# Kernel tuning notes

Hardware: AMD Instinct MI355X
Metric: run time of the kernel (lower is better)

Reference implementation:

```python
import jax, jax.numpy as jnp
import numpy as np

B, N, H, A, S = 8, 8192, 256, 64, 32  # batch, nodes, hidden, annotation, sub_graphs


def _mysoftmax(x):
    # exp, zero out where x <= 0, normalize over last dim, nan (0/0) -> 0
    x_exp = jnp.where(x > 0, jnp.exp(x), 0.0)
    part = jnp.sum(x_exp, axis=-1, keepdims=True)
    # safe divide: where partition == 0 the faithful result after nan_to_num is 0
    return jnp.where(part > 0, x_exp / jnp.where(part > 0, part, 1.0), 0.0)


def setup_inputs() -> dict:
    key = jax.random.key(0)
    k1, k2, k3, k4, k5, k6 = jax.random.split(key, 6)
    x = jax.random.normal(k1, (B, N, H + A), dtype=jnp.float32)
    node_map = jax.random.uniform(k2, (B, S, N), dtype=jnp.float32)
    lim = 1.0 / np.sqrt(H + A)
    Wi = jax.random.uniform(k3, (H, H + A), minval=-lim, maxval=lim, dtype=jnp.float32)
    bi = jax.random.uniform(k4, (H,), minval=-lim, maxval=lim, dtype=jnp.float32)
    Wj = jax.random.uniform(k5, (H, H + A), minval=-lim, maxval=lim, dtype=jnp.float32)
    bj = jax.random.uniform(k6, (H,), minval=-lim, maxval=lim, dtype=jnp.float32)
    return {"x": x, "node_map": node_map, "Wi": Wi, "bi": bi, "Wj": Wj, "bj": bj}


def reference(x, node_map, Wi, bi, Wj, bj):
    # gated node features: sigmoid(fc_i(x)) * tanh(fc_j(x))  -> [B, N, H]
    x_sigm = jax.nn.sigmoid(jnp.einsum('bnf,hf->bnh', x, Wi) + bi)
    x_tanh = jnp.tanh(jnp.einsum('bnf,hf->bnh', x, Wj) + bj)
    x_all = x_sigm * x_tanh
    # per-node L2 norm -> [B, 1, N]
    x_norm = jnp.linalg.norm(x_all, axis=-1)[:, None, :]
    # scaled subgraph map and masked softmax over nodes -> [B, S, N]
    weight = _mysoftmax(node_map * x_norm)
    # weighted sum over nodes (replaces [B,S,N,H] broadcast) -> [B, S, H]
    pooled = jnp.einsum('bsn,bnh->bsh', weight, x_all)
    return jnp.tanh(pooled), weight[..., None]
```

## Files before the change

### kernel.cpp

```cpp
#include <hip/hip_runtime.h>
#include <cstdint>
#include <cstddef>

typedef unsigned short u16;
typedef unsigned int   u32;
using short8 = __attribute__((ext_vector_type(8))) short;
using f32x4  = __attribute__((ext_vector_type(4))) float;

#define NB    8
#define NN    8192
#define HH    256
#define FF    320
#define SS    32
#define NROWS 65536
#define NCH   64

__device__ __forceinline__ u16 f2bf(float f) {
    union { float f; u32 u; } v; v.f = f;
    u32 r = v.u + 0x7fffu + ((v.u >> 16) & 1u);
    return (u16)(r >> 16);
}
__device__ __forceinline__ u32 pk2h(float lo, float hi) {
    union { float f; u32 u; } a, b; a.f = lo; b.f = hi;
    return __builtin_amdgcn_perm(b.u + 0x8000u, a.u + 0x8000u, 0x07060302u);
}
__device__ __forceinline__ short8 pack8(float4 a, float4 b) {
    union { u32 u[4]; short8 s; } r;
    r.u[0] = pk2h(a.x, a.y); r.u[1] = pk2h(a.z, a.w);
    r.u[2] = pk2h(b.x, b.y); r.u[3] = pk2h(b.z, b.w);
    return r.s;
}

__global__ __launch_bounds__(256) void prep_w(const float* __restrict__ Wi,
                                              const float* __restrict__ Wj,
                                              u16* __restrict__ Wb,
                                              float* __restrict__ normsq) {
    int idx = blockIdx.x * 256 + threadIdx.x;
    float v = (idx < 81920) ? Wi[idx] : Wj[idx - 81920];
    Wb[idx] = f2bf(v);
    if (idx < NROWS) normsq[idx] = 0.f;
}

__global__ __launch_bounds__(512, 4) void gemm_gate(
    const float* __restrict__ x, const u16* __restrict__ Wb,
    const float* __restrict__ bi, const float* __restrict__ bj,
    u16* __restrict__ xa, float* __restrict__ normsq)
{
    __shared__ u16 lB[5 * 8192];

    const int bx   = blockIdx.x;
    const int xcd  = bx & 7;
    const int ht   = (bx >> 3) & 3;
    const int slot = bx >> 5;
    const int mb   = xcd + slot * 8;
    const int m0   = mb * 256;
    const int h0   = ht * 64;
    const int b_idx = m0 >> 13;
    const int n0    = m0 & 8191;

    const int tid  = threadIdx.x;
    const int w    = tid >> 6;
    const int lane = tid & 63;
    const int quad = lane >> 4;
    const int l15  = lane & 15;

    {
        const int rsub = lane >> 3;
        const int kg   = (lane & 7) ^ rsub;
        #pragma unroll
        for (int kt = 0; kt < 5; ++kt) {
            #pragma unroll
            for (int j = 0; j < 2; ++j) {
                int sl  = w * 2 + j;
                int row = sl * 8 + rsub;
                int mat = row >> 6, hl = row & 63;
                const u16* gsrc = Wb + mat * 81920 + (size_t)(h0 + hl) * FF + kt * 64 + kg * 8;
                u16* ldst = &lB[kt * 8192 + sl * 512];
                __builtin_amdgcn_global_load_lds(
                    (const __attribute__((address_space(1))) void*)gsrc,
                    (__attribute__((address_space(3))) void*)ldst, 16, 0, 0);
            }
        }
    }

    const float* xb = x + (size_t)(m0 + w * 32 + l15) * FF + quad * 8;

    f32x4 acc[8][2];
    #pragma unroll
    for (int a = 0; a < 8; ++a)
        #pragma unroll
        for (int m = 0; m < 2; ++m) acc[a][m] = (f32x4){0.f, 0.f, 0.f, 0.f};

    float4 pre[3][2][2];
    #pragma unroll
    for (int s = 0; s < 2; ++s)
        #pragma unroll
        for (int mt = 0; mt < 2; ++mt) {
            pre[s][mt][0] = *reinterpret_cast<const float4*>(xb + mt * 16 * FF + s * 32);
            pre[s][mt][1] = *reinterpret_cast<const float4*>(xb + mt * 16 * FF + s * 32 + 4);
        }

    __syncthreads();

    #pragma unroll
    for (int ks = 0; ks < 10; ++ks) {
        const int kt  = ks >> 1, kk = ks & 1;
        const int cur = ks % 3;
        if (ks < 8) {
            const int nx = (ks + 2) % 3;
            const int f  = (ks + 2) * 32;
            #pragma unroll
            for (int mt = 0; mt < 2; ++mt) {
                pre[nx][mt][0] = *reinterpret_cast<const float4*>(xb + mt * 16 * FF + f);
                pre[nx][mt][1] = *reinterpret_cast<const float4*>(xb + mt * 16 * FF + f + 4);
            }
        }
        short8 af0 = pack8(pre[cur][0][0], pre[cur][0][1]);
        short8 af1 = pack8(pre[cur][1][0], pre[cur][1][1]);
        #pragma unroll
        for (int mn = 0; mn < 8; ++mn) {
            int c = mn * 16 + l15;
            short8 bv = *reinterpret_cast<const short8*>(
                &lB[kt * 8192 + c * 64 + (((kk * 4 + quad) ^ (c & 7)) << 3)]);
            acc[mn][0] = __builtin_amdgcn_mfma_f32_16x16x32_bf16(af0, bv, acc[mn][0], 0, 0, 0);
            acc[mn][1] = __builtin_amdgcn_mfma_f32_16x16x32_bf16(af1, bv, acc[mn][1], 0, 0, 0);
        }
    }

    float s0[2][4];
    #pragma unroll
    for (int mt = 0; mt < 2; ++mt)
        #pragma unroll
        for (int r = 0; r < 4; ++r) s0[mt][r] = 0.f;

    #pragma unroll
    for (int hq = 0; hq < 4; ++hq) {
        int h = h0 + hq * 16 + l15;
        float bi_v = bi[h], bj_v = bj[h];
        #pragma unroll
        for (int mt = 0; mt < 2; ++mt) {
            float xall[4];
            #pragma unroll
            for (int r = 0; r < 4; ++r) {
                float yi = acc[hq][mt][r] + bi_v;
                float yj = acc[hq + 4][mt][r] + bj_v;
                float sg = 1.f / (1.f + __expf(-yi));
                float e2 = __expf(-2.f * yj);
                float th = (1.f - e2) / (1.f + e2);
                float xv = sg * th;
                xall[r] = xv;
                s0[mt][r] += xv * xv;
            }
            uint2 pk;
            pk.x = pk2h(xall[0], xall[1]);
            pk.y = pk2h(xall[2], xall[3]);
            size_t o = (size_t)b_idx * ((size_t)HH * NN) + (size_t)h * NN
                     + (size_t)(n0 + w * 32 + mt * 16 + quad * 4);
            *reinterpret_cast<uint2*>(&xa[o]) = pk;
        }
    }
    #pragma unroll
    for (int m = 1; m <= 8; m <<= 1) {
        #pragma unroll
        for (int mt = 0; mt < 2; ++mt)
            #pragma unroll
            for (int r = 0; r < 4; ++r)
                s0[mt][r] += __shfl_xor(s0[mt][r], m, 64);
    }
    if (l15 == 0) {
        #pragma unroll
        for (int mt = 0; mt < 2; ++mt)
            #pragma unroll
            for (int r = 0; r < 4; ++r)
                atomicAdd(&normsq[m0 + w * 32 + mt * 16 + quad * 4 + r], s0[mt][r]);
    }
}

__global__ __launch_bounds__(1024) void softmax_k(
    const float* __restrict__ nm, const float* __restrict__ normsq,
    float* __restrict__ out1)
{
    __shared__ float red[16];
    int bs = blockIdx.x;
    int b  = bs >> 5;
    const float* src = nm + (size_t)bs * NN;
    float* dst       = out1 + (size_t)bs * NN;
    const float* ns  = normsq + (size_t)b * NN;
    int tid = threadIdx.x;
    float e[8];
    float sum = 0.f;
    #pragma unroll
    for (int i = 0; i < 8; ++i) {
        int n = i * 1024 + tid;
        float logit = src[n] * sqrtf(ns[n]);
        float v = (logit > 0.f) ? __expf(logit) : 0.f;
        e[i] = v;
        sum += v;
    }
    #pragma unroll
    for (int m = 1; m <= 32; m <<= 1) sum += __shfl_xor(sum, m, 64);
    int w = tid >> 6, lane = tid & 63;
    if (lane == 0) red[w] = sum;
    __syncthreads();
    float part = 0.f;
    #pragma unroll
    for (int j = 0; j < 16; ++j) part += red[j];
    float inv = (part > 0.f) ? (1.f / part) : 0.f;
    #pragma unroll
    for (int i = 0; i < 8; ++i) dst[i * 1024 + tid] = e[i] * inv;
}

__global__ __launch_bounds__(256) void pooled_k(
    const u16* __restrict__ xa, const float* __restrict__ wgt,
    float* __restrict__ part)
{
    __shared__ u16 lw[32 * 136];
    int bx = blockIdx.x;
    int b  = bx >> 6, c = bx & 63;
    int n0 = c * 128;
    int tid = threadIdx.x, w = tid >> 6, lane = tid & 63, quad = lane >> 4, l15 = lane & 15;

    const u16* ab = xa + (size_t)b * ((size_t)HH * NN) + n0;

    short8 av[2][4];
    #pragma unroll
    for (int htl = 0; htl < 4; ++htl) {
        int h = w * 64 + htl * 16 + l15;
        av[0][htl] = *reinterpret_cast<const short8*>(ab + (size_t)h * NN + quad * 8);
    }

    {
        int s  = tid >> 3;
        int jq = (tid & 7) * 16;
        const float* src = wgt + (size_t)(b * SS + s) * NN + n0 + jq;
        #pragma unroll
        for (int q = 0; q < 4; ++q) {
            float4 v = *reinterpret_cast<const float4*>(src + q * 4);
            uint2 pk;
            pk.x = pk2h(v.x, v.y);
            pk.y = pk2h(v.z, v.w);
            *reinterpret_cast<uint2*>(&lw[s * 136 + jq + q * 4]) = pk;
        }
    }
    __syncthreads();

    f32x4 acc[4][2];
    #pragma unroll
    for (int a = 0; a < 4; ++a)
        #pragma unroll
        for (int s = 0; s < 2; ++s) acc[a][s] = (f32x4){0.f, 0.f, 0.f, 0.f};

    #pragma unroll
    for (int ks = 0; ks < 4; ++ks) {
        const int cur = ks & 1, nxt = cur ^ 1;
        if (ks < 3) {
            #pragma unroll
            for (int htl = 0; htl < 4; ++htl) {
                int h = w * 64 + htl * 16 + l15;
                av[nxt][htl] = *reinterpret_cast<const short8*>(
                    ab + (size_t)h * NN + (ks + 1) * 32 + quad * 8);
            }
        }
        #pragma unroll
        for (int st = 0; st < 2; ++st) {
            int s = st * 16 + l15;
            short8 bv = *reinterpret_cast<const short8*>(&lw[s * 136 + ks * 32 + quad * 8]);
            #pragma unroll
            for (int htl = 0; htl < 4; ++htl)
                acc[htl][st] = __builtin_amdgcn_mfma_f32_16x16x32_bf16(av[cur][htl], bv, acc[htl][st], 0, 0, 0);
        }
    }
    float* pb = part + (size_t)(b * NCH + c) * 8192;
    #pragma unroll
    for (int htl = 0; htl < 4; ++htl) {
        #pragma unroll
        for (int st = 0; st < 2; ++st) {
            int h = w * 64 + htl * 16 + quad * 4;
            int s = st * 16 + l15;
            *reinterpret_cast<f32x4*>(&pb[s * 256 + h]) = acc[htl][st];
        }
    }
}

__global__ __launch_bounds__(256) void reduce_tanh(const float* __restrict__ part,
                                                   float* __restrict__ out0)
{
    int gid = blockIdx.x * 256 + threadIdx.x;
    int b = gid >> 13, r = gid & 8191;
    const float* p = part + (size_t)b * NCH * 8192 + r;
    float s = 0.f;
    #pragma unroll
    for (int c = 0; c < NCH; ++c) s += p[(size_t)c * 8192];
    out0[gid] = tanhf(s);
}

extern "C" void kernel_launch(void* const* d_in, const int* in_sizes, int n_in,
                              void* d_out, int out_size, void* d_ws, size_t ws_size,
                              hipStream_t stream) {
    const float* x  = (const float*)d_in[0];
    const float* nm = (const float*)d_in[1];
    const float* Wi = (const float*)d_in[2];
    const float* bi = (const float*)d_in[3];
    const float* Wj = (const float*)d_in[4];
    const float* bj = (const float*)d_in[5];
    float* out0 = (float*)d_out;
    float* out1 = out0 + NB * SS * HH;

    char* ws = (char*)d_ws;
    u16*   Wb     = (u16*)ws;
    u16*   xa     = (u16*)(ws + 327680);
    float* normsq = (float*)(ws + 327680 + 33554432);
    float* part   = (float*)(ws + 327680 + 33554432 + 262144);

    prep_w     <<<640,  256, 0, stream>>>(Wi, Wj, Wb, normsq);
    gemm_gate  <<<1024, 512, 0, stream>>>(x, Wb, bi, bj, xa, normsq);
    softmax_k  <<<256, 1024, 0, stream>>>(nm, normsq, out1);
    pooled_k   <<<512,  256, 0, stream>>>(xa, out1, part);
    reduce_tanh<<<256,  256, 0, stream>>>(part, out0);
}
```

Before: 214.9 us.

## Double gemm M-tile per block and replace normsq atomics with per-tile partials

Each gemm block now computes 512 rows instead of 256 (4 M sub-tiles per wave), halving the grid and the number of times each block reloads the weight tile into LDS. This raises reuse of each B fragment read from LDS across four MFMAs. The per-row squared-norm is written as four per-h-tile partials instead of atomics, and softmax sums them, which also removes the zeroing pass in prep_w. The cost is higher register pressure from doubled accumulators and prefetch buffers, possibly lowering occupancy. The partial buffer reuses the pooled partial workspace, which is safe only because softmax finishes before pooled_k writes it.

```diff
diff --git a/kernel.cpp b/kernel.cpp
--- a/kernel.cpp
+++ b/kernel.cpp
@@ -33,18 +33,16 @@
 
 __global__ __launch_bounds__(256) void prep_w(const float* __restrict__ Wi,
                                               const float* __restrict__ Wj,
-                                              u16* __restrict__ Wb,
-                                              float* __restrict__ normsq) {
+                                              u16* __restrict__ Wb) {
     int idx = blockIdx.x * 256 + threadIdx.x;
     float v = (idx < 81920) ? Wi[idx] : Wj[idx - 81920];
     Wb[idx] = f2bf(v);
-    if (idx < NROWS) normsq[idx] = 0.f;
 }
 
 __global__ __launch_bounds__(512, 4) void gemm_gate(
     const float* __restrict__ x, const u16* __restrict__ Wb,
     const float* __restrict__ bi, const float* __restrict__ bj,
-    u16* __restrict__ xa, float* __restrict__ normsq)
+    u16* __restrict__ xa, float* __restrict__ normsq_p)
 {
     __shared__ u16 lB[5 * 8192];
 
@@ -53,7 +51,7 @@
     const int ht   = (bx >> 3) & 3;
     const int slot = bx >> 5;
     const int mb   = xcd + slot * 8;
-    const int m0   = mb * 256;
+    const int m0   = mb * 512;
     const int h0   = ht * 64;
     const int b_idx = m0 >> 13;
     const int n0    = m0 & 8191;
@@ -83,19 +81,19 @@
         }
     }
 
-    const float* xb = x + (size_t)(m0 + w * 32 + l15) * FF + quad * 8;
-
-    f32x4 acc[8][2];
+    const float* xb = x + (size_t)(m0 + w * 64 + l15) * FF + quad * 8;
+
+    f32x4 acc[8][4];
     #pragma unroll
     for (int a = 0; a < 8; ++a)
         #pragma unroll
-        for (int m = 0; m < 2; ++m) acc[a][m] = (f32x4){0.f, 0.f, 0.f, 0.f};
-
-    float4 pre[3][2][2];
+        for (int m = 0; m < 4; ++m) acc[a][m] = (f32x4){0.f, 0.f, 0.f, 0.f};
+
+    float4 pre[3][4][2];
     #pragma unroll
     for (int s = 0; s < 2; ++s)
         #pragma unroll
-        for (int mt = 0; mt < 2; ++mt) {
+        for (int mt = 0; mt < 4; ++mt) {
             pre[s][mt][0] = *reinterpret_cast<const float4*>(xb + mt * 16 * FF + s * 32);
             pre[s][mt][1] = *reinterpret_cast<const float4*>(xb + mt * 16 * FF + s * 32 + 4);
         }
@@ -110,26 +108,29 @@
             const int nx = (ks + 2) % 3;
             const int f  = (ks + 2) * 32;
             #pragma unroll
-            for (int mt = 0; mt < 2; ++mt) {
+            for (int mt = 0; mt < 4; ++mt) {
                 pre[nx][mt][0] = *reinterpret_cast<const float4*>(xb + mt * 16 * FF + f);
                 pre[nx][mt][1] = *reinterpret_cast<const float4*>(xb + mt * 16 * FF + f + 4);
             }
         }
-        short8 af0 = pack8(pre[cur][0][0], pre[cur][0][1]);
-        short8 af1 = pack8(pre[cur][1][0], pre[cur][1][1]);
+        short8 af[4];
+        #pragma unroll
+        for (int mt = 0; mt < 4; ++mt)
+            af[mt] = pack8(pre[cur][mt][0], pre[cur][mt][1]);
         #pragma unroll
         for (int mn = 0; mn < 8; ++mn) {
             int c = mn * 16 + l15;
             short8 bv = *reinterpret_cast<const short8*>(
                 &lB[kt * 8192 + c * 64 + (((kk * 4 + quad) ^ (c & 7)) << 3)]);
-            acc[mn][0] = __builtin_amdgcn_mfma_f32_16x16x32_bf16(af0, bv, acc[mn][0], 0, 0, 0);
-            acc[mn][1] = __builtin_amdgcn_mfma_f32_16x16x32_bf16(af1, bv, acc[mn][1], 0, 0, 0);
-        }
-    }
-
-    float s0[2][4];
-    #pragma unroll
-    for (int mt = 0; mt < 2; ++mt)
+            #pragma unroll
+            for (int mt = 0; mt < 4; ++mt)
+                acc[mn][mt] = __builtin_amdgcn_mfma_f32_16x16x32_bf16(af[mt], bv, acc[mn][mt], 0, 0, 0);
+        }
+    }
+
+    float s0[4][4];
+    #pragma unroll
+    for (int mt = 0; mt < 4; ++mt)
         #pragma unroll
         for (int r = 0; r < 4; ++r) s0[mt][r] = 0.f;
 
@@ -138,7 +139,7 @@
         int h = h0 + hq * 16 + l15;
         float bi_v = bi[h], bj_v = bj[h];
         #pragma unroll
-        for (int mt = 0; mt < 2; ++mt) {
+        for (int mt = 0; mt < 4; ++mt) {
             float xall[4];
             #pragma unroll
             for (int r = 0; r < 4; ++r) {
@@ -155,29 +156,29 @@
             pk.x = pk2h(xall[0], xall[1]);
             pk.y = pk2h(xall[2], xall[3]);
             size_t o = (size_t)b_idx * ((size_t)HH * NN) + (size_t)h * NN
-                     + (size_t)(n0 + w * 32 + mt * 16 + quad * 4);
+                     + (size_t)(n0 + w * 64 + mt * 16 + quad * 4);
             *reinterpret_cast<uint2*>(&xa[o]) = pk;
         }
     }
     #pragma unroll
     for (int m = 1; m <= 8; m <<= 1) {
         #pragma unroll
-        for (int mt = 0; mt < 2; ++mt)
+        for (int mt = 0; mt < 4; ++mt)
             #pragma unroll
             for (int r = 0; r < 4; ++r)
                 s0[mt][r] += __shfl_xor(s0[mt][r], m, 64);
     }
     if (l15 == 0) {
         #pragma unroll
-        for (int mt = 0; mt < 2; ++mt)
+        for (int mt = 0; mt < 4; ++mt)
             #pragma unroll
             for (int r = 0; r < 4; ++r)
-                atomicAdd(&normsq[m0 + w * 32 + mt * 16 + quad * 4 + r], s0[mt][r]);
+                normsq_p[ht * NROWS + m0 + w * 64 + mt * 16 + quad * 4 + r] = s0[mt][r];
     }
 }
 
 __global__ __launch_bounds__(1024) void softmax_k(
-    const float* __restrict__ nm, const float* __restrict__ normsq,
+    const float* __restrict__ nm, const float* __restrict__ normsq_p,
     float* __restrict__ out1)
 {
     __shared__ float red[16];
@@ -185,14 +186,15 @@
     int b  = bs >> 5;
     const float* src = nm + (size_t)bs * NN;
     float* dst       = out1 + (size_t)bs * NN;
-    const float* ns  = normsq + (size_t)b * NN;
+    const float* ns  = normsq_p + (size_t)b * NN;
     int tid = threadIdx.x;
     float e[8];
     float sum = 0.f;
     #pragma unroll
     for (int i = 0; i < 8; ++i) {
         int n = i * 1024 + tid;
-        float logit = src[n] * sqrtf(ns[n]);
+        float nsq = ns[n] + ns[n + NROWS] + ns[n + 2 * NROWS] + ns[n + 3 * NROWS];
+        float logit = src[n] * sqrtf(nsq);
         float v = (logit > 0.f) ? __expf(logit) : 0.f;
         e[i] = v;
         sum += v;
@@ -307,14 +309,14 @@
     float* out1 = out0 + NB * SS * HH;
 
     char* ws = (char*)d_ws;
-    u16*   Wb     = (u16*)ws;
-    u16*   xa     = (u16*)(ws + 327680);
-    float* normsq = (float*)(ws + 327680 + 33554432);
-    float* part   = (float*)(ws + 327680 + 33554432 + 262144);
-
-    prep_w     <<<640,  256, 0, stream>>>(Wi, Wj, Wb, normsq);
-    gemm_gate  <<<1024, 512, 0, stream>>>(x, Wb, bi, bj, xa, normsq);
-    softmax_k  <<<256, 1024, 0, stream>>>(nm, normsq, out1);
+    u16*   Wb       = (u16*)ws;
+    u16*   xa       = (u16*)(ws + 327680);
+    float* part     = (float*)(ws + 327680 + 33554432);
+    float* normsq_p = part;
+
+    prep_w     <<<640,  256, 0, stream>>>(Wi, Wj, Wb);
+    gemm_gate  <<<512,  512, 0, stream>>>(x, Wb, bi, bj, xa, normsq_p);
+    softmax_k  <<<256, 1024, 0, stream>>>(nm, normsq_p, out1);
     pooled_k   <<<512,  256, 0, stream>>>(xa, out1, part);
     reduce_tanh<<<256,  256, 0, stream>>>(part, out0);
 }
```

After: 502.4 us. 2.34x slower.

## Pre-cast x to bf16 in a separate pass and replace norm atomics with partial sums

Applied to the files above, without the earlier changes.

Adds a cast_x kernel that converts x to bf16 in workspace so the GEMM reads half-width A operands, with a deeper prefetch ring and no per-tile packing. The squared-norm accumulation becomes per-h-tile partial stores that softmax sums, which removes the atomics and the zeroing in prep_w. The extra pass costs a full read of x plus a bf16 write and reread. It runs only when the workspace is large enough; otherwise an fp32-input fallback GEMM is used.

```diff
diff --git a/kernel.cpp b/kernel.cpp
--- a/kernel.cpp
+++ b/kernel.cpp
@@ -33,18 +33,28 @@
 
 __global__ __launch_bounds__(256) void prep_w(const float* __restrict__ Wi,
                                               const float* __restrict__ Wj,
-                                              u16* __restrict__ Wb,
-                                              float* __restrict__ normsq) {
+                                              u16* __restrict__ Wb) {
     int idx = blockIdx.x * 256 + threadIdx.x;
     float v = (idx < 81920) ? Wi[idx] : Wj[idx - 81920];
     Wb[idx] = f2bf(v);
-    if (idx < NROWS) normsq[idx] = 0.f;
-}
-
-__global__ __launch_bounds__(512, 4) void gemm_gate(
-    const float* __restrict__ x, const u16* __restrict__ Wb,
+}
+
+__global__ __launch_bounds__(256) void cast_x(const float* __restrict__ x,
+                                              u16* __restrict__ xb) {
+    int t = blockIdx.x * 256 + threadIdx.x;
+    #pragma unroll
+    for (int i = 0; i < 4; ++i) {
+        size_t g = (size_t)i * 655360 + t;
+        float4 a = *reinterpret_cast<const float4*>(x + g * 8);
+        float4 b = *reinterpret_cast<const float4*>(x + g * 8 + 4);
+        *reinterpret_cast<short8*>(xb + g * 8) = pack8(a, b);
+    }
+}
+
+__global__ __launch_bounds__(512, 4) void gemm_gate_pre(
+    const u16* __restrict__ xbg, const u16* __restrict__ Wb,
     const float* __restrict__ bi, const float* __restrict__ bj,
-    u16* __restrict__ xa, float* __restrict__ normsq)
+    u16* __restrict__ xa, float* __restrict__ normsq_p)
 {
     __shared__ u16 lB[5 * 8192];
 
@@ -83,7 +93,8 @@
         }
     }
 
-    const float* xb = x + (size_t)(m0 + w * 32 + l15) * FF + quad * 8;
+    const u16* xr0 = xbg + (size_t)(m0 + w * 32 + l15) * FF + quad * 8;
+    const u16* xr1 = xr0 + 16 * FF;
 
     f32x4 acc[8][2];
     #pragma unroll
@@ -91,39 +102,31 @@
         #pragma unroll
         for (int m = 0; m < 2; ++m) acc[a][m] = (f32x4){0.f, 0.f, 0.f, 0.f};
 
-    float4 pre[3][2][2];
-    #pragma unroll
-    for (int s = 0; s < 2; ++s)
-        #pragma unroll
-        for (int mt = 0; mt < 2; ++mt) {
-            pre[s][mt][0] = *reinterpret_cast<const float4*>(xb + mt * 16 * FF + s * 32);
-            pre[s][mt][1] = *reinterpret_cast<const float4*>(xb + mt * 16 * FF + s * 32 + 4);
-        }
+    short8 af[4][2];
+    #pragma unroll
+    for (int s = 0; s < 3; ++s) {
+        af[s][0] = *reinterpret_cast<const short8*>(xr0 + s * 32);
+        af[s][1] = *reinterpret_cast<const short8*>(xr1 + s * 32);
+    }
 
     __syncthreads();
 
     #pragma unroll
     for (int ks = 0; ks < 10; ++ks) {
         const int kt  = ks >> 1, kk = ks & 1;
-        const int cur = ks % 3;
-        if (ks < 8) {
-            const int nx = (ks + 2) % 3;
-            const int f  = (ks + 2) * 32;
-            #pragma unroll
-            for (int mt = 0; mt < 2; ++mt) {
-                pre[nx][mt][0] = *reinterpret_cast<const float4*>(xb + mt * 16 * FF + f);
-                pre[nx][mt][1] = *reinterpret_cast<const float4*>(xb + mt * 16 * FF + f + 4);
-            }
-        }
-        short8 af0 = pack8(pre[cur][0][0], pre[cur][0][1]);
-        short8 af1 = pack8(pre[cur][1][0], pre[cur][1][1]);
+        const int cur = ks & 3;
+        if (ks < 7) {
+            const int nx = (ks + 3) & 3;
+            af[nx][0] = *reinterpret_cast<const short8*>(xr0 + (ks + 3) * 32);
+            af[nx][1] = *reinterpret_cast<const short8*>(xr1 + (ks + 3) * 32);
+        }
         #pragma unroll
         for (int mn = 0; mn < 8; ++mn) {
             int c = mn * 16 + l15;
             short8 bv = *reinterpret_cast<const short8*>(
                 &lB[kt * 8192 + c * 64 + (((kk * 4 + quad) ^ (c & 7)) << 3)]);
-            acc[mn][0] = __builtin_amdgcn_mfma_f32_16x16x32_bf16(af0, bv, acc[mn][0], 0, 0, 0);
-            acc[mn][1] = __builtin_amdgcn_mfma_f32_16x16x32_bf16(af1, bv, acc[mn][1], 0, 0, 0);
+            acc[mn][0] = __builtin_amdgcn_mfma_f32_16x16x32_bf16(af[cur][0], bv, acc[mn][0], 0, 0, 0);
+            acc[mn][1] = __builtin_amdgcn_mfma_f32_16x16x32_bf16(af[cur][1], bv, acc[mn][1], 0, 0, 0);
         }
     }
 
@@ -172,12 +175,147 @@
         for (int mt = 0; mt < 2; ++mt)
             #pragma unroll
             for (int r = 0; r < 4; ++r)
-                atomicAdd(&normsq[m0 + w * 32 + mt * 16 + quad * 4 + r], s0[mt][r]);
+                normsq_p[ht * NROWS + m0 + w * 32 + mt * 16 + quad * 4 + r] = s0[mt][r];
+    }
+}
+
+__global__ __launch_bounds__(512, 4) void gemm_gate_f32(
+    const float* __restrict__ x, const u16* __restrict__ Wb,
+    const float* __restrict__ bi, const float* __restrict__ bj,
+    u16* __restrict__ xa, float* __restrict__ normsq_p)
+{
+    __shared__ u16 lB[5 * 8192];
+
+    const int bx   = blockIdx.x;
+    const int xcd  = bx & 7;
+    const int ht   = (bx >> 3) & 3;
+    const int slot = bx >> 5;
+    const int mb   = xcd + slot * 8;
+    const int m0   = mb * 256;
+    const int h0   = ht * 64;
+    const int b_idx = m0 >> 13;
+    const int n0    = m0 & 8191;
+
+    const int tid  = threadIdx.x;
+    const int w    = tid >> 6;
+    const int lane = tid & 63;
+    const int quad = lane >> 4;
+    const int l15  = lane & 15;
+
+    {
+        const int rsub = lane >> 3;
+        const int kg   = (lane & 7) ^ rsub;
+        #pragma unroll
+        for (int kt = 0; kt < 5; ++kt) {
+            #pragma unroll
+            for (int j = 0; j < 2; ++j) {
+                int sl  = w * 2 + j;
+                int row = sl * 8 + rsub;
+                int mat = row >> 6, hl = row & 63;
+                const u16* gsrc = Wb + mat * 81920 + (size_t)(h0 + hl) * FF + kt * 64 + kg * 8;
+                u16* ldst = &lB[kt * 8192 + sl * 512];
+                __builtin_amdgcn_global_load_lds(
+                    (const __attribute__((address_space(1))) void*)gsrc,
+                    (__attribute__((address_space(3))) void*)ldst, 16, 0, 0);
+            }
+        }
+    }
+
+    const float* xb = x + (size_t)(m0 + w * 32 + l15) * FF + quad * 8;
+
+    f32x4 acc[8][2];
+    #pragma unroll
+    for (int a = 0; a < 8; ++a)
+        #pragma unroll
+        for (int m = 0; m < 2; ++m) acc[a][m] = (f32x4){0.f, 0.f, 0.f, 0.f};
+
+    float4 pre[3][2][2];
+    #pragma unroll
+    for (int s = 0; s < 2; ++s)
+        #pragma unroll
+        for (int mt = 0; mt < 2; ++mt) {
+            pre[s][mt][0] = *reinterpret_cast<const float4*>(xb + mt * 16 * FF + s * 32);
+            pre[s][mt][1] = *reinterpret_cast<const float4*>(xb + mt * 16 * FF + s * 32 + 4);
+        }
+
+    __syncthreads();
+
+    #pragma unroll
+    for (int ks = 0; ks < 10; ++ks) {
+        const int kt  = ks >> 1, kk = ks & 1;
+        const int cur = ks % 3;
+        if (ks < 8) {
+            const int nx = (ks + 2) % 3;
+            const int f  = (ks + 2) * 32;
+            #pragma unroll
+            for (int mt = 0; mt < 2; ++mt) {
+                pre[nx][mt][0] = *reinterpret_cast<const float4*>(xb + mt * 16 * FF + f);
+                pre[nx][mt][1] = *reinterpret_cast<const float4*>(xb + mt * 16 * FF + f + 4);
+            }
+        }
+        short8 af0 = pack8(pre[cur][0][0], pre[cur][0][1]);
+        short8 af1 = pack8(pre[cur][1][0], pre[cur][1][1]);
+        #pragma unroll
+        for (int mn = 0; mn < 8; ++mn) {
+            int c = mn * 16 + l15;
+            short8 bv = *reinterpret_cast<const short8*>(
+                &lB[kt * 8192 + c * 64 + (((kk * 4 + quad) ^ (c & 7)) << 3)]);
+            acc[mn][0] = __builtin_amdgcn_mfma_f32_16x16x32_bf16(af0, bv, acc[mn][0], 0, 0, 0);
+            acc[mn][1] = __builtin_amdgcn_mfma_f32_16x16x32_bf16(af1, bv, acc[mn][1], 0, 0, 0);
+        }
+    }
+
+    float s0[2][4];
+    #pragma unroll
+    for (int mt = 0; mt < 2; ++mt)
+        #pragma unroll
+        for (int r = 0; r < 4; ++r) s0[mt][r] = 0.f;
+
+    #pragma unroll
+    for (int hq = 0; hq < 4; ++hq) {
+        int h = h0 + hq * 16 + l15;
+        float bi_v = bi[h], bj_v = bj[h];
+        #pragma unroll
+        for (int mt = 0; mt < 2; ++mt) {
+            float xall[4];
+            #pragma unroll
+            for (int r = 0; r < 4; ++r) {
+                float yi = acc[hq][mt][r] + bi_v;
+                float yj = acc[hq + 4][mt][r] + bj_v;
+                float sg = 1.f / (1.f + __expf(-yi));
+                float e2 = __expf(-2.f * yj);
+                float th = (1.f - e2) / (1.f + e2);
+                float xv = sg * th;
+                xall[r] = xv;
+                s0[mt][r] += xv * xv;
+            }
+            uint2 pk;
+            pk.x = pk2h(xall[0], xall[1]);
+            pk.y = pk2h(xall[2], xall[3]);
+            size_t o = (size_t)b_idx * ((size_t)HH * NN) + (size_t)h * NN
+                     + (size_t)(n0 + w * 32 + mt * 16 + quad * 4);
+            *reinterpret_cast<uint2*>(&xa[o]) = pk;
+        }
+    }
+    #pragma unroll
+    for (int m = 1; m <= 8; m <<= 1) {
+        #pragma unroll
+        for (int mt = 0; mt < 2; ++mt)
+            #pragma unroll
+            for (int r = 0; r < 4; ++r)
+                s0[mt][r] += __shfl_xor(s0[mt][r], m, 64);
+    }
+    if (l15 == 0) {
+        #pragma unroll
+        for (int mt = 0; mt < 2; ++mt)
+            #pragma unroll
+            for (int r = 0; r < 4; ++r)
+                normsq_p[ht * NROWS + m0 + w * 32 + mt * 16 + quad * 4 + r] = s0[mt][r];
     }
 }
 
 __global__ __launch_bounds__(1024) void softmax_k(
-    const float* __restrict__ nm, const float* __restrict__ normsq,
+    const float* __restrict__ nm, const float* __restrict__ normsq_p,
     float* __restrict__ out1)
 {
     __shared__ float red[16];
@@ -185,14 +323,15 @@
     int b  = bs >> 5;
     const float* src = nm + (size_t)bs * NN;
     float* dst       = out1 + (size_t)bs * NN;
-    const float* ns  = normsq + (size_t)b * NN;
+    const float* ns  = normsq_p + (size_t)b * NN;
     int tid = threadIdx.x;
     float e[8];
     float sum = 0.f;
     #pragma unroll
     for (int i = 0; i < 8; ++i) {
         int n = i * 1024 + tid;
-        float logit = src[n] * sqrtf(ns[n]);
+        float nsq = ns[n] + ns[n + NROWS] + ns[n + 2 * NROWS] + ns[n + 3 * NROWS];
+        float logit = src[n] * sqrtf(nsq);
         float v = (logit > 0.f) ? __expf(logit) : 0.f;
         e[i] = v;
         sum += v;
@@ -307,14 +446,22 @@
     float* out1 = out0 + NB * SS * HH;
 
     char* ws = (char*)d_ws;
-    u16*   Wb     = (u16*)ws;
-    u16*   xa     = (u16*)(ws + 327680);
-    float* normsq = (float*)(ws + 327680 + 33554432);
-    float* part   = (float*)(ws + 327680 + 33554432 + 262144);
-
-    prep_w     <<<640,  256, 0, stream>>>(Wi, Wj, Wb, normsq);
-    gemm_gate  <<<1024, 512, 0, stream>>>(x, Wb, bi, bj, xa, normsq);
-    softmax_k  <<<256, 1024, 0, stream>>>(nm, normsq, out1);
+    size_t off = 0;
+    u16*   Wb       = (u16*)(ws + off);  off += 327680;
+    u16*   xa       = (u16*)(ws + off);  off += 33554432;
+    float* normsq_p = (float*)(ws + off); off += 1048576;
+    float* part     = (float*)(ws + off); off += 16777216;
+    u16*   xb       = (u16*)(ws + off);
+    const size_t need_fast = off + 41943040;
+
+    prep_w<<<640, 256, 0, stream>>>(Wi, Wj, Wb);
+    if (ws_size >= need_fast) {
+        cast_x       <<<2560, 256, 0, stream>>>(x, xb);
+        gemm_gate_pre<<<1024, 512, 0, stream>>>(xb, Wb, bi, bj, xa, normsq_p);
+    } else {
+        gemm_gate_f32<<<1024, 512, 0, stream>>>(x, Wb, bi, bj, xa, normsq_p);
+    }
+    softmax_k  <<<256, 1024, 0, stream>>>(nm, normsq_p, out1);
     pooled_k   <<<512,  256, 0, stream>>>(xa, out1, part);
     reduce_tanh<<<256,  256, 0, stream>>>(part, out0);
 }
```

New measurement: 215.0 us. About the same (+0.0%).
